# Optimization experiments

Measured on AMD Instinct MI355X. Metric: run time of the kernel, lower is better.

Reference implementation:

```python
import jax, jax.numpy as jnp
import numpy as np

S = 7; B = 2; C = 20
IMG_W = 448.0; IMG_H = 448.0
CONF_THRES = 0.5; NMS_THRES = 0.5; IOU_THRES = [0.5]
N = S * S  # 49 boxes per image (one responsible box per cell)
BATCH = 4096


def setup_inputs() -> dict:
    key = jax.random.key(0)
    k1, k2 = jax.random.split(key)
    target = jax.random.uniform(k1, (BATCH, S, S, B * 5 + C), dtype=jnp.float32)
    output = jax.random.normal(k2, (BATCH, S, S, B * 5 + C), dtype=jnp.float32)
    return {"target": target, "output": output}


def _decode(coords):
    # coords: [b,S,S,4] cell-normalized (x,y,w,h) -> xyxy pixel boxes [b,S,S,4]
    gw, gh = IMG_W / S, IMG_H / S
    jx = jnp.arange(S, dtype=coords.dtype)[None, None, :, None]  # column index -> cx
    iy = jnp.arange(S, dtype=coords.dtype)[None, :, None, None]  # row index    -> cy
    cx = (coords[..., 0:1] + jx) * gw
    cy = (coords[..., 1:2] + iy) * gh
    w = coords[..., 2:3] * IMG_W
    h = coords[..., 3:4] * IMG_H
    return jnp.concatenate([cx - w / 2, cy - h / 2, cx + w / 2, cy + h / 2], axis=-1)


def _pairwise_iou(a, b):
    # a: [M,4], b: [K,4] xyxy -> [M,K] IoU (torchvision box_iou semantics)
    lt = jnp.maximum(a[:, None, :2], b[None, :, :2])
    rb = jnp.minimum(a[:, None, 2:], b[None, :, 2:])
    wh = jnp.clip(rb - lt, 0.0)
    inter = wh[..., 0] * wh[..., 1]
    area_a = (a[:, 2] - a[:, 0]) * (a[:, 3] - a[:, 1])
    area_b = (b[:, 2] - b[:, 0]) * (b[:, 3] - b[:, 1])
    return inter / (area_a[:, None] + area_b[None, :] - inter)


def _per_image(ob, oc, ocls, tb, tconf, tcls):
    # Sort preds by conf desc (batched_nms returns score-descending keep order)
    order = jnp.argsort(-oc)
    b_s, c_s, k_s = ob[order], oc[order], ocls[order]
    # class-aware greedy NMS over the 49 boxes
    iou_pp = _pairwise_iou(b_s, b_s)
    sup = (iou_pp > NMS_THRES) & (k_s[:, None] == k_s[None, :])
    idx = jnp.arange(N)
    def nms_body(suppressed, i):
        active = ~suppressed[i]
        suppressed = suppressed | (active & sup[i] & (idx > i))
        return suppressed, active
    _, keep = jax.lax.scan(nms_body, jnp.zeros((N,), bool), idx)
    valid_p = keep & (c_s > CONF_THRES)
    valid_g = tconf > CONF_THRES
    # best same-class GT per pred (max_iou starts at 0 in original; -1 sentinel OK since thr>0)
    cand = (k_s[:, None] == tcls[None, :]) & valid_g[None, :]
    miou = jnp.where(cand, _pairwise_iou(b_s, tb), -1.0)
    return k_s, valid_p, jnp.max(miou, axis=-1), jnp.argmax(miou, axis=-1), valid_g


def _match(mx, best, valid_p, thr):
    # greedy TP/FP assignment over preds in conf-desc order, per image
    def body(matched, i):
        hit = valid_p[i] & (mx[i] > thr) & (~matched[best[i]])
        matched = matched.at[best[i]].set(matched[best[i]] | hit)
        return matched, hit
    _, tp = jax.lax.scan(body, jnp.zeros((N,), bool), jnp.arange(N))
    return tp


def reference(target, output):
    D = B * 5 + C
    target = target.reshape(-1, S, S, D)
    output = jax.nn.sigmoid(output.reshape(-1, S, S, D))
    bsz = output.shape[0]
    # ground-truth decode
    tconf = target[..., 4].reshape(bsz, N)
    tcls = jnp.argmax(target[..., B * 5:], axis=-1).reshape(bsz, N)
    tb = _decode(target[..., 0:4]).reshape(bsz, N, 4)
    # prediction decode: responsible box = max-conf box per cell
    confs = jnp.stack([output[..., b * 5 + 4] for b in range(B)], axis=-1)  # [b,S,S,B]
    oc = jnp.max(confs, axis=-1).reshape(bsz, N)
    resp = jnp.argmax(confs, axis=-1)
    coords = sum((resp == b)[..., None] * output[..., b * 5:b * 5 + 4] for b in range(B))
    ob = _decode(coords).reshape(bsz, N, 4)
    ocls = jnp.argmax(output[..., B * 5:], axis=-1).reshape(bsz, N)

    k_s, valid_p, mx, best, valid_g = jax.vmap(_per_image)(ob, oc, ocls, tb, tconf, tcls)

    # flatten in (image, conf-desc) order == original pred_boxes order
    cls_f = k_s.reshape(-1)
    vp_f = valid_p.reshape(-1)
    gt_count = jax.ops.segment_sum(valid_g.reshape(-1).astype(jnp.float32),
                                   tcls.reshape(-1), num_segments=C)  # [C]
    mask = (cls_f[None, :] == jnp.arange(C)[:, None]) & vp_f[None, :]  # [C, bsz*N]

    aps = []
    for thr in IOU_THRES:
        tp = jax.vmap(_match, in_axes=(0, 0, 0, None))(mx, best, valid_p, thr)
        tp = tp.reshape(-1).astype(jnp.float32)
        # masked entries keep cum values constant -> contribute 0 to trapz
        tpc = jnp.cumsum(jnp.where(mask, tp[None, :], 0.0), axis=1)
        fpc = jnp.cumsum(jnp.where(mask, 1.0 - tp[None, :], 0.0), axis=1)
        recall = tpc / (gt_count[:, None] + 1e-6)
        prec = tpc / (tpc + fpc + 1e-6)
        r = jnp.concatenate([jnp.zeros((C, 1), recall.dtype), recall], axis=1)
        p = jnp.concatenate([jnp.ones((C, 1), prec.dtype), prec], axis=1)
        ap = jnp.sum((r[:, 1:] - r[:, :-1]) * (p[:, 1:] + p[:, :-1]) * 0.5, axis=1)
        has = gt_count > 0  # classes with no GT are skipped in original
        n_has = jnp.maximum(jnp.sum(has.astype(jnp.float32)), 1.0)
        aps.append(jnp.sum(jnp.where(has, ap, 0.0)) / n_has)
    return sum(aps) / len(aps)
```

## Files before the change

kernel.cpp:

```cpp
#include <hip/hip_runtime.h>
#include <stdint.h>

#pragma clang fp contract(off)

#define NCELL 49
#define NCLS  20
#define NSEG  16

struct Box { float x1, y1, x2, y2; };

__device__ __forceinline__ float sigmoid_ref(float x) {
#pragma clang fp contract(off)
  float z = expf(-fabsf(x));
  float num = (x >= 0.0f) ? 1.0f : z;
  return num / (1.0f + z);
}

__device__ __forceinline__ float iou_box(Box a, Box b) {
#pragma clang fp contract(off)
  float lx = fmaxf(a.x1, b.x1);
  float ly = fmaxf(a.y1, b.y1);
  float rx = fminf(a.x2, b.x2);
  float ry = fminf(a.y2, b.y2);
  float w = fmaxf(rx - lx, 0.0f);
  float h = fmaxf(ry - ly, 0.0f);
  float inter = w * h;
  float aa = (a.x2 - a.x1) * (a.y2 - a.y1);
  float ab = (b.x2 - b.x1) * (b.y2 - b.y1);
  return inter / (aa + ab - inter);
}

__device__ __forceinline__ bool iou_gt_half(Box a, Box b) {
#pragma clang fp contract(off)
  float lx = fmaxf(a.x1, b.x1);
  float ly = fmaxf(a.y1, b.y1);
  float rx = fminf(a.x2, b.x2);
  float ry = fminf(a.y2, b.y2);
  float w = fmaxf(rx - lx, 0.0f);
  float h = fmaxf(ry - ly, 0.0f);
  float inter = w * h;
  float aa = (a.x2 - a.x1) * (a.y2 - a.y1);
  float ab = (b.x2 - b.x1) * (b.y2 - b.y1);
  float u = aa + ab - inter;
  return inter > 0.5f * u;
}

__device__ __forceinline__ unsigned mbcnt64(unsigned long long m) {
  return __builtin_amdgcn_mbcnt_hi((unsigned)(m >> 32),
         __builtin_amdgcn_mbcnt_lo((unsigned)m, 0u));
}
#define WSYNC() __builtin_amdgcn_wave_barrier()

__global__ __launch_bounds__(128) void k_per_image(
    const float* __restrict__ target, const float* __restrict__ output,
    uint8_t* __restrict__ entries, unsigned* __restrict__ gtseg,
    unsigned* __restrict__ totals, int batch, int segimg)
{
#pragma clang fp contract(off)
  __shared__ float4   pbox [2][64];
  __shared__ int2     pcc  [2][64];
  __shared__ float4   gboxC[2][64];
  __shared__ int      gorig[2][64];
  __shared__ float    ctab [2][64];
  __shared__ int      claim[2][64];
  __shared__ unsigned phist[2][NCLS];

  int tid = threadIdx.x;
  int lane = tid & 63;
  int wv = tid >> 6;
  int img = blockIdx.x * 2 + wv;
  if (img >= batch) return;
  bool a = (lane < NCELL);
  int seg = img / segimg;

  if (lane < NCLS) phist[wv][lane] = 0u;
  claim[wv][lane] = 64;

  float fjx = (float)(lane % 7), fiy = (float)(lane / 7);

  float ov[30], tv[30];
  if (a) {
    const float2* O2 = (const float2*)(output + (size_t)img * 1470 + lane * 30);
    const float2* T2 = (const float2*)(target + (size_t)img * 1470 + lane * 30);
#pragma unroll
    for (int i = 0; i < 15; ++i) { float2 o = O2[i]; ov[2*i] = o.x; ov[2*i+1] = o.y; }
#pragma unroll
    for (int i = 0; i < 15; ++i) { float2 t = T2[i]; tv[2*i] = t.x; tv[2*i+1] = t.y; }
  } else {
#pragma unroll
    for (int i = 0; i < 30; ++i) { ov[i] = 0.0f; tv[i] = 0.0f; }
  }

  {
    float myc = -1.0f; int myk = 0; float px1 = 0, py1 = 0, px2 = 0, py2 = 0;
    if (a) {
      float x4 = ov[4], x9 = ov[9];
      float xm = fmaxf(x4, x9);
      float xc = ov[10], xr = -3.0e38f; int kk = 0;
#pragma unroll
      for (int c = 1; c < NCLS; ++c) {
        float v = ov[10 + c];
        bool gt = v > xc;
        float nr = gt ? xc : fmaxf(xr, v);
        kk = gt ? c : kk;
        xc = gt ? v : xc;
        xr = nr;
      }
      bool slowK = (xc - xr) < fmaxf(1e-5f, 4e-6f * exp2f(xc * 1.44269504f));
      bool slowR = fabsf(x4 - x9) < fmaxf(1e-5f, 4e-6f * exp2f(xm * 1.44269504f));
      int resp = (x9 > x4) ? 1 : 0;
      myc = sigmoid_ref(xm);
      myk = kk;
      if (slowK || slowR) {
        float s0 = sigmoid_ref(x4);
        float s1 = sigmoid_ref(x9);
        myc = fmaxf(s0, s1);
        resp = (s1 > s0) ? 1 : 0;
        float obv = sigmoid_ref(ov[10]); myk = 0;
#pragma unroll
        for (int c = 1; c < NCLS; ++c) {
          float v = sigmoid_ref(ov[10 + c]);
          if (v > obv) { obv = v; myk = c; }
        }
      }
      float bx = resp ? ov[5] : ov[0];
      float by = resp ? ov[6] : ov[1];
      float bw = resp ? ov[7] : ov[2];
      float bh = resp ? ov[8] : ov[3];
      float x  = sigmoid_ref(bx);
      float y  = sigmoid_ref(by);
      float ww = sigmoid_ref(bw);
      float hh = sigmoid_ref(bh);
      float cx = (x + fjx) * 64.0f, cy = (y + fiy) * 64.0f;
      float W = ww * 448.0f, H = hh * 448.0f;
      px1 = cx - W * 0.5f; py1 = cy - H * 0.5f;
      px2 = cx + W * 0.5f; py2 = cy + H * 0.5f;
    }
    ctab[wv][lane] = myc;
    WSYNC();
    int r = 0;
#pragma unroll
    for (int j = 0; j < NCELL; ++j) {
      float cj = ctab[wv][j];
      r += (cj > myc) || (cj == myc && j < lane);
    }
    r = a ? r : lane;
    pbox[wv][r] = make_float4(px1, py1, px2, py2);
    pcc [wv][r] = make_int2(myk, __float_as_int(myc));
  }

  int mystartR = 0, myendR = 0;
  unsigned gcnt_mine = 0;
  int gclsv = 0; bool gval = false;
  float4 gb4;
  {
    float tbv = tv[10];
#pragma unroll
    for (int c = 1; c < NCLS; ++c) { float v = tv[10 + c]; if (v > tbv) { tbv = v; gclsv = c; } }
    gval = a && (tv[4] > 0.5f);
    float cx = (tv[0] + fjx) * 64.0f, cy = (tv[1] + fiy) * 64.0f;
    float w2 = tv[2] * 448.0f, h2 = tv[3] * 448.0f;
    gb4 = make_float4(cx - w2 * 0.5f, cy - h2 * 0.5f,
                      cx + w2 * 0.5f, cy + h2 * 0.5f);
  }

  WSYNC();
  float4 sb4 = pbox[wv][lane];
  int2 cc = pcc[wv][lane];
  Box myS; myS.x1 = sb4.x; myS.y1 = sb4.y; myS.x2 = sb4.z; myS.y2 = sb4.w;
  int scls = cc.x; float sconf = __int_as_float(cc.y);

  unsigned long long mymask = 0;
  {
    int base = 0, mypos = -1;
#pragma unroll
    for (int c = 0; c < NCLS; ++c) {
      unsigned long long mc = __ballot(gval && (gclsv == c));
      unsigned long long pc2 = __ballot(a && (scls == c));
      int cnt = (int)__popcll(mc);
      bool mine = (scls == c);
      if (mine) { mystartR = base; myendR = base + cnt; }
      mymask = mine ? pc2 : mymask;
      if (gval && gclsv == c) mypos = base + (int)mbcnt64(mc);
      if (lane == c) gcnt_mine = (unsigned)cnt;
      base += cnt;
    }
    if (mypos >= 0) {
      gboxC[wv][mypos] = gb4;
      gorig[wv][mypos] = lane;
    }
    if (lane < NCLS && gcnt_mine) atomicAdd(&gtseg[seg * 32 + lane], gcnt_mine);
  }
  if (!a) { mystartR = 0; myendR = 0; }
  WSYNC();

  float mx = -1.0f; int best = 0;
  for (int g = mystartR; g < myendR; ++g) {
    float4 b4 = gboxC[wv][g];
    int og = gorig[wv][g];
    Box bg; bg.x1 = b4.x; bg.y1 = b4.y; bg.x2 = b4.z; bg.y2 = b4.w;
    float v = iou_box(myS, bg);
    bool upd = (v > mx);
    mx = upd ? v : mx;
    best = upd ? og : best;
  }

  unsigned long long jm = a ? ((mymask >> (lane + 1)) << (lane + 1)) : 0ull;
  unsigned long long row = 0;
  while (jm) {
    int j = (int)__builtin_ctzll(jm);
    jm &= jm - 1;
    float4 b4 = pbox[wv][j];
    Box bj; bj.x1 = b4.x; bj.y1 = b4.y; bj.x2 = b4.z; bj.y2 = b4.w;
    row |= iou_gt_half(myS, bj) ? (1ull << j) : 0ull;
  }
  unsigned long long anyrow = __ballot(row != 0ull);
  unsigned supbit = 0u;
  while (anyrow) {
    int i = (int)__builtin_ctzll(anyrow);
    anyrow &= anyrow - 1;
    unsigned long long ri = __shfl(row, i, 64);
    unsigned si = __shfl(supbit, i, 64);
    supbit |= (!si && ((ri >> lane) & 1ull)) ? 1u : 0u;
  }
  bool vp = a && (supbit == 0u) && (sconf > 0.5f);

  bool elig = vp && (mx > 0.5f);
  if (elig) atomicMin(&claim[wv][best], lane);
  WSYNC();
  bool hit = elig && (claim[wv][best] == lane);

  if (a) {
    entries[(size_t)img * NCELL + lane] =
        (uint8_t)(scls | (vp ? 32 : 0) | (hit ? 64 : 0));
  }

  unsigned add = (vp ? 0x10000u : 0u) | (hit ? 1u : 0u);
  if (a && add) atomicAdd(&phist[wv][scls], add);
  WSYNC();
  if (lane < NCLS) {
    unsigned pkt = phist[wv][lane];
    if (pkt) atomicAdd(&totals[seg * 32 + lane], pkt);
  }
}

__device__ __forceinline__ unsigned match_mask(unsigned w, unsigned wantx4) {
  unsigned y = (w & 0x3f3f3f3fu) ^ wantx4;
  return ~(y + 0x7f7f7f7fu) & 0x80808080u;
}

__device__ __forceinline__ uint4 load_tile(const uint8_t* entries, int e, int e1, int ne) {
  uint4 w4 = make_uint4(0, 0, 0, 0);
  if (e < e1) {
    int p = e << 4;
    if (p + 16 <= ne) {
      w4 = *(const uint4*)(entries + p);
    } else {
      unsigned ws[4] = {0, 0, 0, 0};
      for (int k = 0; k < ne - p; ++k)
        ws[k >> 2] |= ((unsigned)entries[p + k]) << (8 * (k & 3));
      w4.x = ws[0]; w4.y = ws[1]; w4.z = ws[2]; w4.w = ws[3];
    }
  }
  return w4;
}

__global__ __launch_bounds__(1024) void k_apB_fast(
    const uint8_t* __restrict__ entries, const unsigned* __restrict__ totals,
    const unsigned* __restrict__ gtseg, double* __restrict__ partials,
    unsigned* __restrict__ counter, float* __restrict__ out,
    int ne, int segimg)
{
#pragma clang fp contract(off)
  int c = blockIdx.x / NSEG, s = blockIdx.x % NSEG;
  int tid = threadIdx.x, wid = tid >> 6, lane = tid & 63;
  unsigned gtc = 0;
#pragma unroll
  for (int s2 = 0; s2 < NSEG; ++s2) gtc += gtseg[s2 * 32 + c];
  float g2 = (float)gtc + 1e-6f;
  unsigned wantx4 = (32u + (unsigned)c) * 0x01010101u;

  int nel = (ne + 15) >> 4;
  int segel = segimg * NCELL / 16;
  int se0 = s * segel; if (se0 > nel) se0 = nel;
  int se1 = se0 + segel; if (se1 > nel) se1 = nel;
  int elw = (se1 > se0) ? ((se1 - se0 + 15) >> 4) : 0;
  int e0 = se0 + wid * elw; if (e0 > se1) e0 = se1;
  int e1 = e0 + elw; if (e1 > se1) e1 = se1;

  unsigned long long pk = 0;
  if (lane < s) {
    unsigned t2 = totals[lane * 32 + c];
    pk = ((unsigned long long)(t2 >> 16) << 32) | (unsigned long long)(t2 & 0xffffu);
  }
#pragma unroll
  for (int d = 1; d < 64; d <<= 1) pk += __shfl_xor(pk, d, 64);
  unsigned Jrun = (unsigned)(pk >> 32), Trun = (unsigned)(pk & 0xffffffffull);

  int e = e0 + lane;
  int p = e << 4;
  uint4 w4 = load_tile(entries, e, e1, ne);
  unsigned wsv[4] = {w4.x, w4.y, w4.z, w4.w};
  unsigned mm[4], tm[4];
  unsigned cv = 0, ct = 0;
#pragma unroll
  for (int q = 0; q < 4; ++q) {
    unsigned m = match_mask(wsv[q], wantx4);
    mm[q] = m; tm[q] = m & (wsv[q] << 1);
    cv += __popc(m); ct += __popc(tm[q]);
  }

  unsigned long long tot = ((unsigned long long)cv << 32) | (unsigned long long)ct;
#pragma unroll
  for (int d = 1; d < 64; d <<= 1) tot += __shfl_xor(tot, d, 64);
  __shared__ unsigned long long wt[16];
  __shared__ double wacc[16];
  __shared__ int islast;
  __shared__ float apf_s[NCLS];
  __shared__ unsigned ghas_s[NCLS];
  if (lane == 0) wt[wid] = tot;
  __syncthreads();
  for (int w2 = 0; w2 < wid; ++w2) {
    Jrun += (unsigned)(wt[w2] >> 32);
    Trun += (unsigned)(wt[w2] & 0xffffffffull);
  }

  unsigned jexcl = 0, texcl = 0;
#pragma unroll
  for (int b = 0; b < 5; ++b) {
    unsigned long long mj = __ballot(((cv >> b) & 1u) != 0u);
    unsigned long long mk = __ballot(((ct >> b) & 1u) != 0u);
    jexcl += mbcnt64(mj) << b;
    texcl += mbcnt64(mk) << b;
  }
  unsigned jr = Jrun + jexcl;
  unsigned tr = Trun + texcl;

  double acc = 0.0;
#pragma unroll
  for (int q = 0; q < 4; ++q) {
    unsigned m = mm[q];
    while (m) {
      unsigned bit = (unsigned)__builtin_ctz(m);
      m &= m - 1;
      ++jr;
      if (tm[q] & (1u << bit)) {
        ++tr;
        int pos = p + 4 * q + (int)(bit >> 3);
        float ft = (float)tr, fj = (float)jr;
        float r_cur  = ft / g2;
        float r_prev = (ft - 1.0f) / g2;
        float p_cur  = ft / (fj + 1e-6f);
        float p_prev = (pos == 0) ? 1.0f
                                  : (ft - 1.0f) / ((fj - 1.0f) + 1e-6f);
        acc += (double)((r_cur - r_prev) * (p_cur + p_prev) * 0.5f);
      }
    }
  }

  for (int d = 32; d > 0; d >>= 1) acc += __shfl_down(acc, d, 64);
  if (lane == 0) wacc[wid] = acc;
  __syncthreads();
  if (tid == 0) {
    double bp = 0.0;
#pragma unroll
    for (int w2 = 0; w2 < 16; ++w2) bp += wacc[w2];
    __hip_atomic_store(&partials[blockIdx.x], bp,
                       __ATOMIC_RELEASE, __HIP_MEMORY_SCOPE_AGENT);
    unsigned prev = __hip_atomic_fetch_add(counter, 1u,
                       __ATOMIC_ACQ_REL, __HIP_MEMORY_SCOPE_AGENT);
    islast = (prev == (unsigned)(NCLS * NSEG - 1)) ? 1 : 0;
  }
  __syncthreads();
  if (islast) {
    if (tid < NCLS) {
      double d2 = 0.0;
#pragma unroll
      for (int s2 = 0; s2 < NSEG; ++s2)
        d2 += __hip_atomic_load(&partials[tid * NSEG + s2],
                                __ATOMIC_ACQUIRE, __HIP_MEMORY_SCOPE_AGENT);
      apf_s[tid] = (float)d2;
      unsigned gc = 0;
#pragma unroll
      for (int s2 = 0; s2 < NSEG; ++s2) gc += gtseg[s2 * 32 + tid];
      ghas_s[tid] = gc;
    }
    __syncthreads();
    if (tid == 0) {
      float sf = 0.0f, nf = 0.0f;
      for (int cc = 0; cc < NCLS; ++cc)
        if (ghas_s[cc] > 0) { sf += apf_s[cc]; nf += 1.0f; }
      out[0] = sf / fmaxf(nf, 1.0f);
    }
  }
}

__global__ __launch_bounds__(256) void k_apB(
    const uint8_t* __restrict__ entries, const unsigned* __restrict__ totals,
    const unsigned* __restrict__ gtseg, double* __restrict__ partials,
    unsigned* __restrict__ counter, float* __restrict__ out,
    int ne, int segimg)
{
#pragma clang fp contract(off)
  int c = blockIdx.x / NSEG, s = blockIdx.x % NSEG;
  int tid = threadIdx.x, wid = tid >> 6, lane = tid & 63;
  unsigned gtc = 0;
#pragma unroll
  for (int s2 = 0; s2 < NSEG; ++s2) gtc += gtseg[s2 * 32 + c];
  float g2 = (float)gtc + 1e-6f;
  unsigned wantx4 = (32u + (unsigned)c) * 0x01010101u;

  int nel = (ne + 15) >> 4;
  int segel = segimg * NCELL / 16;
  int se0 = s * segel; if (se0 > nel) se0 = nel;
  int se1 = se0 + segel; if (se1 > nel) se1 = nel;
  int elw = (se1 > se0) ? ((se1 - se0 + 3) >> 2) : 0;
  int e0 = se0 + wid * elw; if (e0 > se1) e0 = se1;
  int e1 = e0 + elw; if (e1 > se1) e1 = se1;
  int ntile = (e1 > e0) ? ((e1 - e0 + 63) >> 6) : 0;

  unsigned long long pk = 0;
  if (lane < s) {
    unsigned t2 = totals[lane * 32 + c];
    pk = ((unsigned long long)(t2 >> 16) << 32) | (unsigned long long)(t2 & 0xffffu);
  }
#pragma unroll
  for (int d = 1; d < 64; d <<= 1) pk += __shfl_xor(pk, d, 64);
  unsigned Jrun = (unsigned)(pk >> 32), Trun = (unsigned)(pk & 0xffffffffull);

  unsigned mv = 0, mt = 0;
  for (int t = 0; t < ntile; ++t) {
    uint4 w4 = load_tile(entries, e0 + t * 64 + lane, e1, ne);
    unsigned wsv[4] = {w4.x, w4.y, w4.z, w4.w};
#pragma unroll
    for (int q = 0; q < 4; ++q) {
      unsigned m = match_mask(wsv[q], wantx4);
      mv += __popc(m);
      mt += __popc(m & (wsv[q] << 1));
    }
  }
  unsigned long long tot = ((unsigned long long)mv << 32) | (unsigned long long)mt;
#pragma unroll
  for (int d = 1; d < 64; d <<= 1) tot += __shfl_xor(tot, d, 64);
  __shared__ unsigned long long wt[4];
  __shared__ double wacc[4];
  __shared__ int islast;
  __shared__ float apf_s[NCLS];
  __shared__ unsigned ghas_s[NCLS];
  if (lane == 0) wt[wid] = tot;
  __syncthreads();
  for (int w2 = 0; w2 < wid; ++w2) {
    Jrun += (unsigned)(wt[w2] >> 32);
    Trun += (unsigned)(wt[w2] & 0xffffffffull);
  }

  double acc = 0.0;
  for (int t = 0; t < ntile; ++t) {
    int e = e0 + t * 64 + lane;
    int p = e << 4;
    uint4 w4 = load_tile(entries, e, e1, ne);
    unsigned wsv[4] = {w4.x, w4.y, w4.z, w4.w};
    unsigned mm[4], tm[4];
    unsigned cv = 0, ct = 0;
#pragma unroll
    for (int q = 0; q < 4; ++q) {
      unsigned m = match_mask(wsv[q], wantx4);
      mm[q] = m; tm[q] = m & (wsv[q] << 1);
      cv += __popc(m); ct += __popc(tm[q]);
    }
    unsigned jexcl = 0, texcl = 0, jtt = 0, ttt = 0;
#pragma unroll
    for (int b = 0; b < 5; ++b) {
      unsigned long long mj = __ballot(((cv >> b) & 1u) != 0u);
      unsigned long long mk = __ballot(((ct >> b) & 1u) != 0u);
      jexcl += mbcnt64(mj) << b;
      texcl += mbcnt64(mk) << b;
      jtt   += (unsigned)__popcll(mj) << b;
      ttt   += (unsigned)__popcll(mk) << b;
    }
    unsigned jr = Jrun + jexcl;
    unsigned tr = Trun + texcl;
#pragma unroll
    for (int q = 0; q < 4; ++q) {
      unsigned m = mm[q];
      while (m) {
        unsigned bit = (unsigned)__builtin_ctz(m);
        m &= m - 1;
        ++jr;
        if (tm[q] & (1u << bit)) {
          ++tr;
          int pos = p + 4 * q + (int)(bit >> 3);
          float ft = (float)tr, fj = (float)jr;
          float r_cur  = ft / g2;
          float r_prev = (ft - 1.0f) / g2;
          float p_cur  = ft / (fj + 1e-6f);
          float p_prev = (pos == 0) ? 1.0f
                                    : (ft - 1.0f) / ((fj - 1.0f) + 1e-6f);
          acc += (double)((r_cur - r_prev) * (p_cur + p_prev) * 0.5f);
        }
      }
    }
    Jrun += jtt;
    Trun += ttt;
  }

  for (int d = 32; d > 0; d >>= 1) acc += __shfl_down(acc, d, 64);
  if (lane == 0) wacc[wid] = acc;
  __syncthreads();
  if (tid == 0) {
    double bp = wacc[0] + wacc[1] + wacc[2] + wacc[3];
    __hip_atomic_store(&partials[blockIdx.x], bp,
                       __ATOMIC_RELEASE, __HIP_MEMORY_SCOPE_AGENT);
    unsigned prev = __hip_atomic_fetch_add(counter, 1u,
                       __ATOMIC_ACQ_REL, __HIP_MEMORY_SCOPE_AGENT);
    islast = (prev == (unsigned)(NCLS * NSEG - 1)) ? 1 : 0;
  }
  __syncthreads();
  if (islast) {
    if (tid < NCLS) {
      double d2 = 0.0;
#pragma unroll
      for (int s2 = 0; s2 < NSEG; ++s2)
        d2 += __hip_atomic_load(&partials[tid * NSEG + s2],
                                __ATOMIC_ACQUIRE, __HIP_MEMORY_SCOPE_AGENT);
      apf_s[tid] = (float)d2;
      unsigned gc = 0;
#pragma unroll
      for (int s2 = 0; s2 < NSEG; ++s2) gc += gtseg[s2 * 32 + tid];
      ghas_s[tid] = gc;
    }
    __syncthreads();
    if (tid == 0) {
      float sf = 0.0f, nf = 0.0f;
      for (int cc = 0; cc < NCLS; ++cc)
        if (ghas_s[cc] > 0) { sf += apf_s[cc]; nf += 1.0f; }
      out[0] = sf / fmaxf(nf, 1.0f);
    }
  }
}

extern "C" void kernel_launch(void* const* d_in, const int* in_sizes, int n_in,
                              void* d_out, int out_size, void* d_ws, size_t ws_size,
                              hipStream_t stream) {
  const float* target = (const float*)d_in[0];
  const float* output = (const float*)d_in[1];
  int batch = in_sizes[0] / (NCELL * 30);
  int ne = batch * NCELL;
  int segimg = (((batch + NSEG - 1) / NSEG) + 15) & ~15;

  uint8_t*  entries  = (uint8_t*)d_ws;
  size_t offA = ((size_t)ne + 255) & ~(size_t)255;
  unsigned* totals   = (unsigned*)((char*)d_ws + offA);
  unsigned* gtseg    = (unsigned*)((char*)d_ws + offA + 2048);
  unsigned* counter  = (unsigned*)((char*)d_ws + offA + 4096);
  double*   partials = (double*)((char*)d_ws + offA + 4352);

  (void)hipMemsetAsync((char*)d_ws + offA, 0, 4352, stream);
  k_per_image<<<(batch + 1) / 2, 128, 0, stream>>>(
      target, output, entries, gtseg, totals, batch, segimg);
  int segel = segimg * NCELL / 16;
  if (segel <= 1024) {
    k_apB_fast<<<NCLS * NSEG, 1024, 0, stream>>>(
        entries, totals, gtseg, partials, counter, (float*)d_out, ne, segimg);
  } else {
    k_apB<<<NCLS * NSEG, 256, 0, stream>>>(
        entries, totals, gtseg, partials, counter, (float*)d_out, ne, segimg);
  }
}
```

Baseline: 109.2 us.

## Process two images per wavefront with upfront loads and 256-thread blocks

Each wavefront now handles two images, issuing the global loads for both before computing either, and blocks grow from two to four wavefronts. The intent is more memory-level parallelism per wave and less launch and block overhead, with compute for the second image hiding behind the loads of both. The cost is doubled register arrays (120 floats), which may lower occupancy or cause spills, plus extra shared memory per block.

After: 112.3 us. +2.8%, slower.

```diff
diff --git a/kernel.cpp b/kernel.cpp
--- a/kernel.cpp
+++ b/kernel.cpp
@@ -51,196 +51,208 @@
 }
 #define WSYNC() __builtin_amdgcn_wave_barrier()
 
-__global__ __launch_bounds__(128) void k_per_image(
+__global__ __launch_bounds__(256) void k_per_image(
     const float* __restrict__ target, const float* __restrict__ output,
     uint8_t* __restrict__ entries, unsigned* __restrict__ gtseg,
     unsigned* __restrict__ totals, int batch, int segimg)
 {
 #pragma clang fp contract(off)
-  __shared__ float4   pbox [2][64];
-  __shared__ int2     pcc  [2][64];
-  __shared__ float4   gboxC[2][64];
-  __shared__ int      gorig[2][64];
-  __shared__ float    ctab [2][64];
-  __shared__ int      claim[2][64];
-  __shared__ unsigned phist[2][NCLS];
+  __shared__ float4   pbox [4][64];
+  __shared__ int2     pcc  [4][64];
+  __shared__ float4   gboxC[4][64];
+  __shared__ int      gorig[4][64];
+  __shared__ float    ctab [4][64];
+  __shared__ int      claim[4][64];
+  __shared__ unsigned phist[4][NCLS];
 
   int tid = threadIdx.x;
   int lane = tid & 63;
   int wv = tid >> 6;
-  int img = blockIdx.x * 2 + wv;
-  if (img >= batch) return;
+  int base = (blockIdx.x * 4 + wv) * 2;
+  if (base >= batch) return;
   bool a = (lane < NCELL);
-  int seg = img / segimg;
-
-  if (lane < NCLS) phist[wv][lane] = 0u;
-  claim[wv][lane] = 64;
 
   float fjx = (float)(lane % 7), fiy = (float)(lane / 7);
 
-  float ov[30], tv[30];
-  if (a) {
-    const float2* O2 = (const float2*)(output + (size_t)img * 1470 + lane * 30);
-    const float2* T2 = (const float2*)(target + (size_t)img * 1470 + lane * 30);
-#pragma unroll
-    for (int i = 0; i < 15; ++i) { float2 o = O2[i]; ov[2*i] = o.x; ov[2*i+1] = o.y; }
-#pragma unroll
-    for (int i = 0; i < 15; ++i) { float2 t = T2[i]; tv[2*i] = t.x; tv[2*i+1] = t.y; }
-  } else {
-#pragma unroll
-    for (int i = 0; i < 30; ++i) { ov[i] = 0.0f; tv[i] = 0.0f; }
-  }
-
-  {
-    float myc = -1.0f; int myk = 0; float px1 = 0, py1 = 0, px2 = 0, py2 = 0;
+  float ovb[2][30], tvb[2][30];
+#pragma unroll
+  for (int ii = 0; ii < 2; ++ii) {
+    int img = base + ii;
+    if ((img < batch) && a) {
+      const float2* O2 = (const float2*)(output + (size_t)img * 1470 + lane * 30);
+      const float2* T2 = (const float2*)(target + (size_t)img * 1470 + lane * 30);
+#pragma unroll
+      for (int i = 0; i < 15; ++i) { float2 o = O2[i]; ovb[ii][2*i] = o.x; ovb[ii][2*i+1] = o.y; }
+#pragma unroll
+      for (int i = 0; i < 15; ++i) { float2 t = T2[i]; tvb[ii][2*i] = t.x; tvb[ii][2*i+1] = t.y; }
+    } else {
+#pragma unroll
+      for (int i = 0; i < 30; ++i) { ovb[ii][i] = 0.0f; tvb[ii][i] = 0.0f; }
+    }
+  }
+
+#pragma unroll
+  for (int ii = 0; ii < 2; ++ii) {
+    int img = base + ii;
+    if (img >= batch) continue;
+    int seg = img / segimg;
+
+    if (lane < NCLS) phist[wv][lane] = 0u;
+    claim[wv][lane] = 64;
+    WSYNC();
+
+    {
+      float myc = -1.0f; int myk = 0; float px1 = 0, py1 = 0, px2 = 0, py2 = 0;
+      if (a) {
+        float x4 = ovb[ii][4], x9 = ovb[ii][9];
+        float xm = fmaxf(x4, x9);
+        float xc = ovb[ii][10], xr = -3.0e38f; int kk = 0;
+#pragma unroll
+        for (int c = 1; c < NCLS; ++c) {
+          float v = ovb[ii][10 + c];
+          bool gt = v > xc;
+          float nr = gt ? xc : fmaxf(xr, v);
+          kk = gt ? c : kk;
+          xc = gt ? v : xc;
+          xr = nr;
+        }
+        bool slowK = (xc - xr) < fmaxf(1e-5f, 4e-6f * exp2f(xc * 1.44269504f));
+        bool slowR = fabsf(x4 - x9) < fmaxf(1e-5f, 4e-6f * exp2f(xm * 1.44269504f));
+        int resp = (x9 > x4) ? 1 : 0;
+        myc = sigmoid_ref(xm);
+        myk = kk;
+        if (slowK || slowR) {
+          float s0 = sigmoid_ref(x4);
+          float s1 = sigmoid_ref(x9);
+          myc = fmaxf(s0, s1);
+          resp = (s1 > s0) ? 1 : 0;
+          float obv = sigmoid_ref(ovb[ii][10]); myk = 0;
+#pragma unroll
+          for (int c = 1; c < NCLS; ++c) {
+            float v = sigmoid_ref(ovb[ii][10 + c]);
+            if (v > obv) { obv = v; myk = c; }
+          }
+        }
+        float bx = resp ? ovb[ii][5] : ovb[ii][0];
+        float by = resp ? ovb[ii][6] : ovb[ii][1];
+        float bw = resp ? ovb[ii][7] : ovb[ii][2];
+        float bh = resp ? ovb[ii][8] : ovb[ii][3];
+        float x  = sigmoid_ref(bx);
+        float y  = sigmoid_ref(by);
+        float ww = sigmoid_ref(bw);
+        float hh = sigmoid_ref(bh);
+        float cx = (x + fjx) * 64.0f, cy = (y + fiy) * 64.0f;
+        float W = ww * 448.0f, H = hh * 448.0f;
+        px1 = cx - W * 0.5f; py1 = cy - H * 0.5f;
+        px2 = cx + W * 0.5f; py2 = cy + H * 0.5f;
+      }
+      ctab[wv][lane] = myc;
+      WSYNC();
+      int r = 0;
+#pragma unroll
+      for (int j = 0; j < NCELL; ++j) {
+        float cj = ctab[wv][j];
+        r += (cj > myc) || (cj == myc && j < lane);
+      }
+      r = a ? r : lane;
+      pbox[wv][r] = make_float4(px1, py1, px2, py2);
+      pcc [wv][r] = make_int2(myk, __float_as_int(myc));
+    }
+
+    int mystartR = 0, myendR = 0;
+    unsigned gcnt_mine = 0;
+    int gclsv = 0; bool gval = false;
+    float4 gb4;
+    {
+      float tbv = tvb[ii][10];
+#pragma unroll
+      for (int c = 1; c < NCLS; ++c) { float v = tvb[ii][10 + c]; if (v > tbv) { tbv = v; gclsv = c; } }
+      gval = a && (tvb[ii][4] > 0.5f);
+      float cx = (tvb[ii][0] + fjx) * 64.0f, cy = (tvb[ii][1] + fiy) * 64.0f;
+      float w2 = tvb[ii][2] * 448.0f, h2 = tvb[ii][3] * 448.0f;
+      gb4 = make_float4(cx - w2 * 0.5f, cy - h2 * 0.5f,
+                        cx + w2 * 0.5f, cy + h2 * 0.5f);
+    }
+
+    WSYNC();
+    float4 sb4 = pbox[wv][lane];
+    int2 cc = pcc[wv][lane];
+    Box myS; myS.x1 = sb4.x; myS.y1 = sb4.y; myS.x2 = sb4.z; myS.y2 = sb4.w;
+    int scls = cc.x; float sconf = __int_as_float(cc.y);
+
+    unsigned long long mymask = 0;
+    {
+      int base2 = 0, mypos = -1;
+#pragma unroll
+      for (int c = 0; c < NCLS; ++c) {
+        unsigned long long mc = __ballot(gval && (gclsv == c));
+        unsigned long long pc2 = __ballot(a && (scls == c));
+        int cnt = (int)__popcll(mc);
+        bool mine = (scls == c);
+        if (mine) { mystartR = base2; myendR = base2 + cnt; }
+        mymask = mine ? pc2 : mymask;
+        if (gval && gclsv == c) mypos = base2 + (int)mbcnt64(mc);
+        if (lane == c) gcnt_mine = (unsigned)cnt;
+        base2 += cnt;
+      }
+      if (mypos >= 0) {
+        gboxC[wv][mypos] = gb4;
+        gorig[wv][mypos] = lane;
+      }
+      if (lane < NCLS && gcnt_mine) atomicAdd(&gtseg[seg * 32 + lane], gcnt_mine);
+    }
+    if (!a) { mystartR = 0; myendR = 0; }
+    WSYNC();
+
+    float mx = -1.0f; int best = 0;
+    for (int g = mystartR; g < myendR; ++g) {
+      float4 b4 = gboxC[wv][g];
+      int og = gorig[wv][g];
+      Box bg; bg.x1 = b4.x; bg.y1 = b4.y; bg.x2 = b4.z; bg.y2 = b4.w;
+      float v = iou_box(myS, bg);
+      bool upd = (v > mx);
+      mx = upd ? v : mx;
+      best = upd ? og : best;
+    }
+
+    unsigned long long jm = a ? ((mymask >> (lane + 1)) << (lane + 1)) : 0ull;
+    unsigned long long row = 0;
+    while (jm) {
+      int j = (int)__builtin_ctzll(jm);
+      jm &= jm - 1;
+      float4 b4 = pbox[wv][j];
+      Box bj; bj.x1 = b4.x; bj.y1 = b4.y; bj.x2 = b4.z; bj.y2 = b4.w;
+      row |= iou_gt_half(myS, bj) ? (1ull << j) : 0ull;
+    }
+    unsigned long long anyrow = __ballot(row != 0ull);
+    unsigned supbit = 0u;
+    while (anyrow) {
+      int i = (int)__builtin_ctzll(anyrow);
+      anyrow &= anyrow - 1;
+      unsigned long long ri = __shfl(row, i, 64);
+      unsigned si = __shfl(supbit, i, 64);
+      supbit |= (!si && ((ri >> lane) & 1ull)) ? 1u : 0u;
+    }
+    bool vp = a && (supbit == 0u) && (sconf > 0.5f);
+
+    bool elig = vp && (mx > 0.5f);
+    if (elig) atomicMin(&claim[wv][best], lane);
+    WSYNC();
+    bool hit = elig && (claim[wv][best] == lane);
+
     if (a) {
-      float x4 = ov[4], x9 = ov[9];
-      float xm = fmaxf(x4, x9);
-      float xc = ov[10], xr = -3.0e38f; int kk = 0;
-#pragma unroll
-      for (int c = 1; c < NCLS; ++c) {
-        float v = ov[10 + c];
-        bool gt = v > xc;
-        float nr = gt ? xc : fmaxf(xr, v);
-        kk = gt ? c : kk;
-        xc = gt ? v : xc;
-        xr = nr;
-      }
-      bool slowK = (xc - xr) < fmaxf(1e-5f, 4e-6f * exp2f(xc * 1.44269504f));
-      bool slowR = fabsf(x4 - x9) < fmaxf(1e-5f, 4e-6f * exp2f(xm * 1.44269504f));
-      int resp = (x9 > x4) ? 1 : 0;
-      myc = sigmoid_ref(xm);
-      myk = kk;
-      if (slowK || slowR) {
-        float s0 = sigmoid_ref(x4);
-        float s1 = sigmoid_ref(x9);
-        myc = fmaxf(s0, s1);
-        resp = (s1 > s0) ? 1 : 0;
-        float obv = sigmoid_ref(ov[10]); myk = 0;
-#pragma unroll
-        for (int c = 1; c < NCLS; ++c) {
-          float v = sigmoid_ref(ov[10 + c]);
-          if (v > obv) { obv = v; myk = c; }
-        }
-      }
-      float bx = resp ? ov[5] : ov[0];
-      float by = resp ? ov[6] : ov[1];
-      float bw = resp ? ov[7] : ov[2];
-      float bh = resp ? ov[8] : ov[3];
-      float x  = sigmoid_ref(bx);
-      float y  = sigmoid_ref(by);
-      float ww = sigmoid_ref(bw);
-      float hh = sigmoid_ref(bh);
-      float cx = (x + fjx) * 64.0f, cy = (y + fiy) * 64.0f;
-      float W = ww * 448.0f, H = hh * 448.0f;
-      px1 = cx - W * 0.5f; py1 = cy - H * 0.5f;
-      px2 = cx + W * 0.5f; py2 = cy + H * 0.5f;
-    }
-    ctab[wv][lane] = myc;
+      entries[(size_t)img * NCELL + lane] =
+          (uint8_t)(scls | (vp ? 32 : 0) | (hit ? 64 : 0));
+    }
+
+    unsigned add = (vp ? 0x10000u : 0u) | (hit ? 1u : 0u);
+    if (a && add) atomicAdd(&phist[wv][scls], add);
     WSYNC();
-    int r = 0;
-#pragma unroll
-    for (int j = 0; j < NCELL; ++j) {
-      float cj = ctab[wv][j];
-      r += (cj > myc) || (cj == myc && j < lane);
-    }
-    r = a ? r : lane;
-    pbox[wv][r] = make_float4(px1, py1, px2, py2);
-    pcc [wv][r] = make_int2(myk, __float_as_int(myc));
-  }
-
-  int mystartR = 0, myendR = 0;
-  unsigned gcnt_mine = 0;
-  int gclsv = 0; bool gval = false;
-  float4 gb4;
-  {
-    float tbv = tv[10];
-#pragma unroll
-    for (int c = 1; c < NCLS; ++c) { float v = tv[10 + c]; if (v > tbv) { tbv = v; gclsv = c; } }
-    gval = a && (tv[4] > 0.5f);
-    float cx = (tv[0] + fjx) * 64.0f, cy = (tv[1] + fiy) * 64.0f;
-    float w2 = tv[2] * 448.0f, h2 = tv[3] * 448.0f;
-    gb4 = make_float4(cx - w2 * 0.5f, cy - h2 * 0.5f,
-                      cx + w2 * 0.5f, cy + h2 * 0.5f);
-  }
-
-  WSYNC();
-  float4 sb4 = pbox[wv][lane];
-  int2 cc = pcc[wv][lane];
-  Box myS; myS.x1 = sb4.x; myS.y1 = sb4.y; myS.x2 = sb4.z; myS.y2 = sb4.w;
-  int scls = cc.x; float sconf = __int_as_float(cc.y);
-
-  unsigned long long mymask = 0;
-  {
-    int base = 0, mypos = -1;
-#pragma unroll
-    for (int c = 0; c < NCLS; ++c) {
-      unsigned long long mc = __ballot(gval && (gclsv == c));
-      unsigned long long pc2 = __ballot(a && (scls == c));
-      int cnt = (int)__popcll(mc);
-      bool mine = (scls == c);
-      if (mine) { mystartR = base; myendR = base + cnt; }
-      mymask = mine ? pc2 : mymask;
-      if (gval && gclsv == c) mypos = base + (int)mbcnt64(mc);
-      if (lane == c) gcnt_mine = (unsigned)cnt;
-      base += cnt;
-    }
-    if (mypos >= 0) {
-      gboxC[wv][mypos] = gb4;
-      gorig[wv][mypos] = lane;
-    }
-    if (lane < NCLS && gcnt_mine) atomicAdd(&gtseg[seg * 32 + lane], gcnt_mine);
-  }
-  if (!a) { mystartR = 0; myendR = 0; }
-  WSYNC();
-
-  float mx = -1.0f; int best = 0;
-  for (int g = mystartR; g < myendR; ++g) {
-    float4 b4 = gboxC[wv][g];
-    int og = gorig[wv][g];
-    Box bg; bg.x1 = b4.x; bg.y1 = b4.y; bg.x2 = b4.z; bg.y2 = b4.w;
-    float v = iou_box(myS, bg);
-    bool upd = (v > mx);
-    mx = upd ? v : mx;
-    best = upd ? og : best;
-  }
-
-  unsigned long long jm = a ? ((mymask >> (lane + 1)) << (lane + 1)) : 0ull;
-  unsigned long long row = 0;
-  while (jm) {
-    int j = (int)__builtin_ctzll(jm);
-    jm &= jm - 1;
-    float4 b4 = pbox[wv][j];
-    Box bj; bj.x1 = b4.x; bj.y1 = b4.y; bj.x2 = b4.z; bj.y2 = b4.w;
-    row |= iou_gt_half(myS, bj) ? (1ull << j) : 0ull;
-  }
-  unsigned long long anyrow = __ballot(row != 0ull);
-  unsigned supbit = 0u;
-  while (anyrow) {
-    int i = (int)__builtin_ctzll(anyrow);
-    anyrow &= anyrow - 1;
-    unsigned long long ri = __shfl(row, i, 64);
-    unsigned si = __shfl(supbit, i, 64);
-    supbit |= (!si && ((ri >> lane) & 1ull)) ? 1u : 0u;
-  }
-  bool vp = a && (supbit == 0u) && (sconf > 0.5f);
-
-  bool elig = vp && (mx > 0.5f);
-  if (elig) atomicMin(&claim[wv][best], lane);
-  WSYNC();
-  bool hit = elig && (claim[wv][best] == lane);
-
-  if (a) {
-    entries[(size_t)img * NCELL + lane] =
-        (uint8_t)(scls | (vp ? 32 : 0) | (hit ? 64 : 0));
-  }
-
-  unsigned add = (vp ? 0x10000u : 0u) | (hit ? 1u : 0u);
-  if (a && add) atomicAdd(&phist[wv][scls], add);
-  WSYNC();
-  if (lane < NCLS) {
-    unsigned pkt = phist[wv][lane];
-    if (pkt) atomicAdd(&totals[seg * 32 + lane], pkt);
+    if (lane < NCLS) {
+      unsigned pkt = phist[wv][lane];
+      if (pkt) atomicAdd(&totals[seg * 32 + lane], pkt);
+    }
+    WSYNC();
   }
 }
 
@@ -556,7 +568,7 @@
   double*   partials = (double*)((char*)d_ws + offA + 4352);
 
   (void)hipMemsetAsync((char*)d_ws + offA, 0, 4352, stream);
-  k_per_image<<<(batch + 1) / 2, 128, 0, stream>>>(
+  k_per_image<<<(batch + 7) / 8, 256, 0, stream>>>(
       target, output, entries, gtseg, totals, batch, segimg);
   int segel = segimg * NCELL / 16;
   if (segel <= 1024) {
```
